# Kernel optimization log

Measured on AMD Instinct MI355X. Metric: run time of the kernel, lower is better.

## Reference

```python
import jax, jax.numpy as jnp
import numpy as np

NHEAD, HEAD_DIM = 10, 10
TEMPERATURE = 1.0
INV_SQRT_HD = np.float32(1.0 / np.sqrt(HEAD_DIM))


def setup_inputs() -> dict:
    key = jax.random.key(0)
    ks = jax.random.split(key, 6)
    B, nhid, L = 4, 128, 1024
    D = NHEAD * HEAD_DIM  # 100
    x = jax.random.normal(ks[0], (B, nhid, L, 1), dtype=jnp.float32)
    edge_matrix = jax.random.randint(ks[1], (B, L, L), 0, 2, dtype=jnp.int32)
    wq_w = jax.random.normal(ks[2], (D, nhid), dtype=jnp.float32) * 0.05
    wq_b = jnp.zeros((D,), jnp.float32)
    wedge_w = jax.random.normal(ks[3], (2 * HEAD_DIM,), dtype=jnp.float32) * 0.1
    wedge_b = jnp.zeros((1,), jnp.float32)
    wo_w = jax.random.normal(ks[4], (nhid, D), dtype=jnp.float32) * 0.05
    wo_b = jnp.zeros((nhid,), jnp.float32)
    return dict(x=x, edge_matrix=edge_matrix, wq_w=wq_w, wq_b=wq_b,
                wedge_w=wedge_w, wedge_b=wedge_b, wo_w=wo_w, wo_b=wo_b)


def reference(x, edge_matrix, wq_w, wq_b, wedge_w, wedge_b, wo_w, wo_b):
    B, nhid, L, _ = x.shape
    # WQ: 1x1 conv == per-position linear over channels
    q = jnp.einsum('bhl,ch->bcl', x[..., 0], wq_w) + wq_b[None, :, None]  # (B, nhead*hd, L)
    # source overwrites k and v with q (WK/WV dead code): k == v == q
    k = q.reshape(B, NHEAD, HEAD_DIM, L).transpose(0, 1, 3, 2)  # (B, nhead, L, hd)
    # WEDGE(Linear(2*hd,1)) over concat[k_i, k_j] == w1.k_i + w2.k_j + b (exact same math,
    # avoids materializing the O(L^2 * 2*hd) a_input tensor)
    s_i = jnp.einsum('bnld,d->bnl', k, wedge_w[:HEAD_DIM])
    s_j = jnp.einsum('bnld,d->bnl', k, wedge_w[HEAD_DIM:])
    alpha = (s_i[:, :, :, None] + s_j[:, :, None, :] + wedge_b[0]) * INV_SQRT_HD  # (B,nhead,L,L)
    alpha = jnp.where(edge_matrix[:, None, :, :] == 0, jnp.float32(-1e15), alpha)
    alpha = jax.nn.softmax(alpha, axis=-1) / TEMPERATURE  # dropout: identity at eval
    att = jnp.einsum('bnij,bnjd->bnid', alpha, k)  # v == k; (B, nhead, L, hd)
    # faithful to torch: raw row-major view(B, -1, L, 1) that scrambles (head,pos) ordering
    att = att.reshape(B, NHEAD * HEAD_DIM, L, 1)
    ret = jnp.einsum('bcl,oc->bol', att[..., 0], wo_w) + wo_b[None, :, None]
    ret = ret[..., None]  # (B, nhid, L, 1)
    return ret, alpha.reshape(B * NHEAD, L, L)
```

## Files before the change

### kernel.cpp

```cpp
#include <hip/hip_runtime.h>

#define BB   4
#define NHID 128
#define LL   1024
#define NH   10
#define HD   10
#define DD   100
#define SCALE 0.31622776601683794f

typedef float vfloat4 __attribute__((ext_vector_type(4)));

__global__ __launch_bounds__(256) void k_qproj(
    const float* __restrict__ x, const float* __restrict__ wq_w,
    const float* __restrict__ wq_b, float* __restrict__ kT) {
  const int l  = blockIdx.x * 256 + threadIdx.x;
  const int c0 = blockIdx.y * 2;
  const int b  = blockIdx.z;
  float acc0 = wq_b[c0], acc1 = wq_b[c0 + 1];
  const float* xb = x + (size_t)b * NHID * LL + l;
  const float* w0 = wq_w + (size_t)c0 * NHID;
  const float* w1 = w0 + NHID;
  #pragma unroll 8
  for (int h = 0; h < NHID; ++h) {
    float xv = xb[(size_t)h * LL];
    acc0 += w0[h] * xv;
    acc1 += w1[h] * xv;
  }
  {
    int c = c0, n = c / HD, d = c % HD;
    kT[(((size_t)(b * NH + n)) * HD + d) * LL + l] = acc0;
  }
  {
    int c = c0 + 1, n = c / HD, d = c % HD;
    kT[(((size_t)(b * NH + n)) * HD + d) * LL + l] = acc1;
  }
}

__global__ __launch_bounds__(256) void k_edgeproj(
    const float* __restrict__ kT, const float* __restrict__ we_w,
    float* __restrict__ esj) {
  const int idx = blockIdx.x * 256 + threadIdx.x;
  const int bn = idx >> 10, l = idx & (LL - 1);
  const float* kp = kT + (size_t)bn * HD * LL + l;
  float s2 = 0.f;
  #pragma unroll
  for (int d = 0; d < HD; ++d) s2 += kp[(size_t)d * LL] * we_w[HD + d];
  esj[idx] = __expf(s2 * SCALE);
}

__global__ __launch_bounds__(512) void k_attn(
    const float* __restrict__ kT, const float* __restrict__ esj,
    const int* __restrict__ edge,
    float* __restrict__ alpha_out, float* __restrict__ att) {
  const int t    = threadIdx.x;
  const int lane = t & 63;
  const int wid  = t >> 6;
  const int blk  = blockIdx.x;
  const int rt   = blk & 31;
  const int bn   = blk >> 5;
  const int b    = bn / NH;
  const int i0   = rt * 32 + wid * 4;

  __shared__ float ksT[HD * LL];
  {
    const float4* src = (const float4*)(kT + (size_t)bn * (HD * LL));
    float4* dst = (float4*)ksT;
    #pragma unroll
    for (int idx = t; idx < (HD * LL) / 4; idx += 512) dst[idx] = src[idx];
  }
  vfloat4 esv[4];
  {
    const vfloat4* sp = (const vfloat4*)(esj + (size_t)bn * LL);
    #pragma unroll
    for (int m = 0; m < 4; ++m) esv[m] = sp[m * 64 + lane];
  }
  __syncthreads();

  const int* ebase = edge + (size_t)b * LL * LL + (size_t)i0 * LL;

  float part[4][HD];
  float denom[4];
  unsigned mask[4];
  #pragma unroll
  for (int r = 0; r < 4; ++r) {
    denom[r] = 0.f; mask[r] = 0u;
    #pragma unroll
    for (int d = 0; d < HD; ++d) part[r][d] = 0.f;
  }
  #pragma unroll
  for (int m = 0; m < 4; ++m) {
    vfloat4 kv[HD];
    const float* kb = ksT + m * 256 + lane * 4;
    #pragma unroll
    for (int d = 0; d < HD; ++d) kv[d] = *(const vfloat4*)(kb + d * LL);
    const vfloat4 es = esv[m];
    #pragma unroll
    for (int r = 0; r < 4; ++r) {
      int4 e = ((const int4*)(ebase + (size_t)r * LL))[m * 64 + lane];
      float ax = e.x ? es.x : 0.f;
      float ay = e.y ? es.y : 0.f;
      float az = e.z ? es.z : 0.f;
      float aw = e.w ? es.w : 0.f;
      mask[r] |= ((e.x ? 1u : 0u) | (e.y ? 2u : 0u) | (e.z ? 4u : 0u) | (e.w ? 8u : 0u)) << (m * 4);
      denom[r] += (ax + ay) + (az + aw);
      #pragma unroll
      for (int d = 0; d < HD; ++d)
        part[r][d] += ax * kv[d].x + ay * kv[d].y + az * kv[d].z + aw * kv[d].w;
    }
  }
  float inv[4];
  #pragma unroll
  for (int r = 0; r < 4; ++r) {
    float s = denom[r];
    #pragma unroll
    for (int sft = 32; sft >= 1; sft >>= 1) s += __shfl_xor(s, sft, 64);
    inv[r] = __builtin_amdgcn_rcpf(s);
  }

  float* ap = alpha_out + ((size_t)bn * LL + i0) * LL;
  #pragma unroll
  for (int m = 0; m < 4; ++m) {
    const vfloat4 es = esv[m];
    #pragma unroll
    for (int r = 0; r < 4; ++r) {
      const unsigned mk = mask[r] >> (m * 4);
      vfloat4 a;
      a.x = (mk & 1u) ? es.x * inv[r] : 0.f;
      a.y = (mk & 2u) ? es.y * inv[r] : 0.f;
      a.z = (mk & 4u) ? es.z * inv[r] : 0.f;
      a.w = (mk & 8u) ? es.w * inv[r] : 0.f;
      vfloat4* dst = (vfloat4*)(ap + (size_t)r * LL) + m * 64 + lane;
      __builtin_nontemporal_store(a, dst);
    }
  }

  const bool b5 = (lane & 32) != 0;
  const bool b4 = (lane & 16) != 0;
  const bool b3 = (lane & 8) != 0;
  const bool b2 = (lane & 4) != 0;
  #pragma unroll
  for (int r = 0; r < 4; ++r) {
    float pv[16];
    #pragma unroll
    for (int d = 0; d < HD; ++d) pv[d] = part[r][d];
    #pragma unroll
    for (int d = HD; d < 16; ++d) pv[d] = 0.f;
    #pragma unroll
    for (int i = 0; i < 8; ++i) {
      float snd = b5 ? pv[i] : pv[i + 8];
      float kp  = b5 ? pv[i + 8] : pv[i];
      pv[i] = kp + __shfl_xor(snd, 32, 64);
    }
    #pragma unroll
    for (int i = 0; i < 4; ++i) {
      float snd = b4 ? pv[i] : pv[i + 4];
      float kp  = b4 ? pv[i + 4] : pv[i];
      pv[i] = kp + __shfl_xor(snd, 16, 64);
    }
    #pragma unroll
    for (int i = 0; i < 2; ++i) {
      float snd = b3 ? pv[i] : pv[i + 2];
      float kp  = b3 ? pv[i + 2] : pv[i];
      pv[i] = kp + __shfl_xor(snd, 8, 64);
    }
    {
      float snd = b2 ? pv[0] : pv[1];
      float kp  = b2 ? pv[1] : pv[0];
      pv[0] = kp + __shfl_xor(snd, 4, 64);
    }
    pv[0] += __shfl_xor(pv[0], 2, 64);
    pv[0] += __shfl_xor(pv[0], 1, 64);
    float g = __shfl(pv[0], lane * 4, 64);
    if (lane < HD)
      att[((size_t)bn * LL + (i0 + r)) * HD + lane] = g * inv[r];
  }
}

__global__ __launch_bounds__(256) void k_out(
    const float* __restrict__ att, const float* __restrict__ wo_w,
    const float* __restrict__ wo_b, float* __restrict__ ret) {
  const int l  = blockIdx.x * 256 + threadIdx.x;
  const int o0 = blockIdx.y * 4;
  const int b  = blockIdx.z;
  const float* ab = att + (size_t)b * (DD * LL);
  float acc[4];
  #pragma unroll
  for (int oo = 0; oo < 4; ++oo) acc[oo] = wo_b[o0 + oo];
  for (int c = 0; c < DD; ++c) {
    float a = ab[(size_t)c * LL + l];
    #pragma unroll
    for (int oo = 0; oo < 4; ++oo) acc[oo] += wo_w[(size_t)(o0 + oo) * DD + c] * a;
  }
  #pragma unroll
  for (int oo = 0; oo < 4; ++oo)
    ret[((size_t)b * NHID + o0 + oo) * LL + l] = acc[oo];
}

extern "C" void kernel_launch(void* const* d_in, const int* in_sizes, int n_in,
                              void* d_out, int out_size, void* d_ws, size_t ws_size,
                              hipStream_t stream) {
  (void)in_sizes; (void)n_in; (void)out_size; (void)ws_size;
  const float* x    = (const float*)d_in[0];
  const int*   edge = (const int*)d_in[1];
  const float* wq_w = (const float*)d_in[2];
  const float* wq_b = (const float*)d_in[3];
  const float* we_w = (const float*)d_in[4];
  const float* wo_w = (const float*)d_in[6];
  const float* wo_b = (const float*)d_in[7];

  float* out       = (float*)d_out;
  float* ret_out   = out;
  float* alpha_out = out + (size_t)BB * NHID * LL;

  float* ws   = (float*)d_ws;
  float* kT   = ws;
  float* esj  = kT + (size_t)BB * NH * HD * LL;
  float* att  = esj + (size_t)BB * NH * LL;

  dim3 g1(LL / 256, DD / 2, BB);
  k_qproj<<<g1, 256, 0, stream>>>(x, wq_w, wq_b, kT);

  k_edgeproj<<<(BB * NH * LL) / 256, 256, 0, stream>>>(kT, we_w, esj);

  k_attn<<<BB * NH * (LL / 32), 512, 0, stream>>>(kT, esj, edge, alpha_out, att);

  dim3 g3(LL / 256, NHID / 4, BB);
  k_out<<<g3, 256, 0, stream>>>(att, wo_w, wo_b, ret_out);
}
```

Before: 255.3 us.

## Process two heads per attention block to reuse edge mask loads

The attention kernel now handles two heads per block. It loads the edge matrix rows once into a bitmask and reuses that mask for both heads, which halves global reads of the large int32 edge tensor. Shared memory per block doubles to 80KB and launch bounds now request 3 blocks per CU, which may reduce occupancy. The Q projection also computes 4 output channels per thread instead of 2, cutting repeated reads of x.

New measurement: 356.3 us. +39.6%, slower.

```diff
diff --git a/kernel.cpp b/kernel.cpp
--- a/kernel.cpp
+++ b/kernel.cpp
@@ -14,25 +14,23 @@
     const float* __restrict__ x, const float* __restrict__ wq_w,
     const float* __restrict__ wq_b, float* __restrict__ kT) {
   const int l  = blockIdx.x * 256 + threadIdx.x;
-  const int c0 = blockIdx.y * 2;
+  const int c0 = blockIdx.y * 4;
   const int b  = blockIdx.z;
-  float acc0 = wq_b[c0], acc1 = wq_b[c0 + 1];
+  float acc[4];
+  #pragma unroll
+  for (int i = 0; i < 4; ++i) acc[i] = wq_b[c0 + i];
   const float* xb = x + (size_t)b * NHID * LL + l;
   const float* w0 = wq_w + (size_t)c0 * NHID;
-  const float* w1 = w0 + NHID;
-  #pragma unroll 8
+  #pragma unroll 4
   for (int h = 0; h < NHID; ++h) {
     float xv = xb[(size_t)h * LL];
-    acc0 += w0[h] * xv;
-    acc1 += w1[h] * xv;
-  }
-  {
-    int c = c0, n = c / HD, d = c % HD;
-    kT[(((size_t)(b * NH + n)) * HD + d) * LL + l] = acc0;
-  }
-  {
-    int c = c0 + 1, n = c / HD, d = c % HD;
-    kT[(((size_t)(b * NH + n)) * HD + d) * LL + l] = acc1;
+    #pragma unroll
+    for (int i = 0; i < 4; ++i) acc[i] += w0[i * NHID + h] * xv;
+  }
+  #pragma unroll
+  for (int i = 0; i < 4; ++i) {
+    int c = c0 + i, n = c / HD, d = c % HD;
+    kT[(((size_t)(b * NH + n)) * HD + d) * LL + l] = acc[i];
   }
 }
 
@@ -48,131 +46,154 @@
   esj[idx] = __expf(s2 * SCALE);
 }
 
-__global__ __launch_bounds__(512) void k_attn(
+__device__ __forceinline__ void pv_reduce_store(
+    float part[4][HD], const float* inv, float* __restrict__ att,
+    int bn, int i0, int lane) {
+  const bool c5 = (lane & 32) != 0;
+  const bool c4 = (lane & 16) != 0;
+  const bool c3 = (lane & 8) != 0;
+  const bool c2 = (lane & 4) != 0;
+  #pragma unroll
+  for (int r = 0; r < 4; ++r) {
+    float pv[16];
+    #pragma unroll
+    for (int d = 0; d < HD; ++d) pv[d] = part[r][d];
+    #pragma unroll
+    for (int d = HD; d < 16; ++d) pv[d] = 0.f;
+    #pragma unroll
+    for (int i = 0; i < 8; ++i) {
+      float snd = c5 ? pv[i] : pv[i + 8];
+      float kp  = c5 ? pv[i + 8] : pv[i];
+      pv[i] = kp + __shfl_xor(snd, 32, 64);
+    }
+    #pragma unroll
+    for (int i = 0; i < 4; ++i) {
+      float snd = c4 ? pv[i] : pv[i + 4];
+      float kp  = c4 ? pv[i + 4] : pv[i];
+      pv[i] = kp + __shfl_xor(snd, 16, 64);
+    }
+    #pragma unroll
+    for (int i = 0; i < 2; ++i) {
+      float snd = c3 ? pv[i] : pv[i + 2];
+      float kp  = c3 ? pv[i + 2] : pv[i];
+      pv[i] = kp + __shfl_xor(snd, 8, 64);
+    }
+    {
+      float snd = c2 ? pv[0] : pv[1];
+      float kp  = c2 ? pv[1] : pv[0];
+      pv[0] = kp + __shfl_xor(snd, 4, 64);
+    }
+    pv[0] += __shfl_xor(pv[0], 2, 64);
+    pv[0] += __shfl_xor(pv[0], 1, 64);
+    float g = __shfl(pv[0], lane * 4, 64);
+    if (lane < HD)
+      att[((size_t)bn * LL + (i0 + r)) * HD + lane] = g * inv[r];
+  }
+}
+
+__global__ __launch_bounds__(512, 3) void k_attn(
     const float* __restrict__ kT, const float* __restrict__ esj,
     const int* __restrict__ edge,
     float* __restrict__ alpha_out, float* __restrict__ att) {
   const int t    = threadIdx.x;
   const int lane = t & 63;
   const int wid  = t >> 6;
-  const int blk  = blockIdx.x;
-  const int rt   = blk & 31;
-  const int bn   = blk >> 5;
-  const int b    = bn / NH;
+  const int rt   = blockIdx.x;
+  const int hp   = blockIdx.y;
+  const int b    = blockIdx.z;
+  const int bn0  = b * NH + hp * 2;
   const int i0   = rt * 32 + wid * 4;
 
-  __shared__ float ksT[HD * LL];
+  __shared__ float ksT2[2 * HD * LL];
   {
-    const float4* src = (const float4*)(kT + (size_t)bn * (HD * LL));
-    float4* dst = (float4*)ksT;
-    #pragma unroll
-    for (int idx = t; idx < (HD * LL) / 4; idx += 512) dst[idx] = src[idx];
-  }
-  vfloat4 esv[4];
+    const float4* src = (const float4*)(kT + (size_t)bn0 * (HD * LL));
+    float4* dst = (float4*)ksT2;
+    #pragma unroll
+    for (int idx = t; idx < (2 * HD * LL) / 4; idx += 512) dst[idx] = src[idx];
+  }
+  vfloat4 esv[2][4];
   {
-    const vfloat4* sp = (const vfloat4*)(esj + (size_t)bn * LL);
-    #pragma unroll
-    for (int m = 0; m < 4; ++m) esv[m] = sp[m * 64 + lane];
+    #pragma unroll
+    for (int h = 0; h < 2; ++h) {
+      const vfloat4* sp = (const vfloat4*)(esj + (size_t)(bn0 + h) * LL);
+      #pragma unroll
+      for (int m = 0; m < 4; ++m) esv[h][m] = sp[m * 64 + lane];
+    }
   }
   __syncthreads();
 
   const int* ebase = edge + (size_t)b * LL * LL + (size_t)i0 * LL;
-
-  float part[4][HD];
-  float denom[4];
-  unsigned mask[4];
-  #pragma unroll
-  for (int r = 0; r < 4; ++r) {
-    denom[r] = 0.f; mask[r] = 0u;
-    #pragma unroll
-    for (int d = 0; d < HD; ++d) part[r][d] = 0.f;
-  }
+  unsigned mask[4] = {0u, 0u, 0u, 0u};
   #pragma unroll
   for (int m = 0; m < 4; ++m) {
-    vfloat4 kv[HD];
-    const float* kb = ksT + m * 256 + lane * 4;
-    #pragma unroll
-    for (int d = 0; d < HD; ++d) kv[d] = *(const vfloat4*)(kb + d * LL);
-    const vfloat4 es = esv[m];
     #pragma unroll
     for (int r = 0; r < 4; ++r) {
       int4 e = ((const int4*)(ebase + (size_t)r * LL))[m * 64 + lane];
-      float ax = e.x ? es.x : 0.f;
-      float ay = e.y ? es.y : 0.f;
-      float az = e.z ? es.z : 0.f;
-      float aw = e.w ? es.w : 0.f;
-      mask[r] |= ((e.x ? 1u : 0u) | (e.y ? 2u : 0u) | (e.z ? 4u : 0u) | (e.w ? 8u : 0u)) << (m * 4);
-      denom[r] += (ax + ay) + (az + aw);
-      #pragma unroll
-      for (int d = 0; d < HD; ++d)
-        part[r][d] += ax * kv[d].x + ay * kv[d].y + az * kv[d].z + aw * kv[d].w;
-    }
-  }
-  float inv[4];
-  #pragma unroll
-  for (int r = 0; r < 4; ++r) {
-    float s = denom[r];
-    #pragma unroll
-    for (int sft = 32; sft >= 1; sft >>= 1) s += __shfl_xor(s, sft, 64);
-    inv[r] = __builtin_amdgcn_rcpf(s);
-  }
-
-  float* ap = alpha_out + ((size_t)bn * LL + i0) * LL;
-  #pragma unroll
-  for (int m = 0; m < 4; ++m) {
-    const vfloat4 es = esv[m];
+      mask[r] |= ((e.x ? 1u : 0u) | (e.y ? 2u : 0u) |
+                  (e.z ? 4u : 0u) | (e.w ? 8u : 0u)) << (m * 4);
+    }
+  }
+
+  #pragma unroll
+  for (int h = 0; h < 2; ++h) {
+    const int bn = bn0 + h;
+    const float* ksT = ksT2 + h * (HD * LL);
+
+    float part[4][HD];
+    float denom[4];
     #pragma unroll
     for (int r = 0; r < 4; ++r) {
-      const unsigned mk = mask[r] >> (m * 4);
-      vfloat4 a;
-      a.x = (mk & 1u) ? es.x * inv[r] : 0.f;
-      a.y = (mk & 2u) ? es.y * inv[r] : 0.f;
-      a.z = (mk & 4u) ? es.z * inv[r] : 0.f;
-      a.w = (mk & 8u) ? es.w * inv[r] : 0.f;
-      vfloat4* dst = (vfloat4*)(ap + (size_t)r * LL) + m * 64 + lane;
-      __builtin_nontemporal_store(a, dst);
-    }
-  }
-
-  const bool b5 = (lane & 32) != 0;
-  const bool b4 = (lane & 16) != 0;
-  const bool b3 = (lane & 8) != 0;
-  const bool b2 = (lane & 4) != 0;
-  #pragma unroll
-  for (int r = 0; r < 4; ++r) {
-    float pv[16];
-    #pragma unroll
-    for (int d = 0; d < HD; ++d) pv[d] = part[r][d];
-    #pragma unroll
-    for (int d = HD; d < 16; ++d) pv[d] = 0.f;
-    #pragma unroll
-    for (int i = 0; i < 8; ++i) {
-      float snd = b5 ? pv[i] : pv[i + 8];
-      float kp  = b5 ? pv[i + 8] : pv[i];
-      pv[i] = kp + __shfl_xor(snd, 32, 64);
-    }
-    #pragma unroll
-    for (int i = 0; i < 4; ++i) {
-      float snd = b4 ? pv[i] : pv[i + 4];
-      float kp  = b4 ? pv[i + 4] : pv[i];
-      pv[i] = kp + __shfl_xor(snd, 16, 64);
-    }
-    #pragma unroll
-    for (int i = 0; i < 2; ++i) {
-      float snd = b3 ? pv[i] : pv[i + 2];
-      float kp  = b3 ? pv[i + 2] : pv[i];
-      pv[i] = kp + __shfl_xor(snd, 8, 64);
-    }
-    {
-      float snd = b2 ? pv[0] : pv[1];
-      float kp  = b2 ? pv[1] : pv[0];
-      pv[0] = kp + __shfl_xor(snd, 4, 64);
-    }
-    pv[0] += __shfl_xor(pv[0], 2, 64);
-    pv[0] += __shfl_xor(pv[0], 1, 64);
-    float g = __shfl(pv[0], lane * 4, 64);
-    if (lane < HD)
-      att[((size_t)bn * LL + (i0 + r)) * HD + lane] = g * inv[r];
+      denom[r] = 0.f;
+      #pragma unroll
+      for (int d = 0; d < HD; ++d) part[r][d] = 0.f;
+    }
+    #pragma unroll
+    for (int m = 0; m < 4; ++m) {
+      vfloat4 kv[HD];
+      const float* kb = ksT + m * 256 + lane * 4;
+      #pragma unroll
+      for (int d = 0; d < HD; ++d) kv[d] = *(const vfloat4*)(kb + d * LL);
+      const vfloat4 es = esv[h][m];
+      #pragma unroll
+      for (int r = 0; r < 4; ++r) {
+        const unsigned mk = mask[r] >> (m * 4);
+        float ax = (mk & 1u) ? es.x : 0.f;
+        float ay = (mk & 2u) ? es.y : 0.f;
+        float az = (mk & 4u) ? es.z : 0.f;
+        float aw = (mk & 8u) ? es.w : 0.f;
+        denom[r] += (ax + ay) + (az + aw);
+        #pragma unroll
+        for (int d = 0; d < HD; ++d)
+          part[r][d] += ax * kv[d].x + ay * kv[d].y + az * kv[d].z + aw * kv[d].w;
+      }
+    }
+    float inv[4];
+    #pragma unroll
+    for (int r = 0; r < 4; ++r) {
+      float s = denom[r];
+      #pragma unroll
+      for (int sft = 32; sft >= 1; sft >>= 1) s += __shfl_xor(s, sft, 64);
+      inv[r] = __builtin_amdgcn_rcpf(s);
+    }
+
+    float* ap = alpha_out + ((size_t)bn * LL + i0) * LL;
+    #pragma unroll
+    for (int m = 0; m < 4; ++m) {
+      const vfloat4 es = esv[h][m];
+      #pragma unroll
+      for (int r = 0; r < 4; ++r) {
+        const unsigned mk = mask[r] >> (m * 4);
+        vfloat4 a;
+        a.x = (mk & 1u) ? es.x * inv[r] : 0.f;
+        a.y = (mk & 2u) ? es.y * inv[r] : 0.f;
+        a.z = (mk & 4u) ? es.z * inv[r] : 0.f;
+        a.w = (mk & 8u) ? es.w * inv[r] : 0.f;
+        vfloat4* dst = (vfloat4*)(ap + (size_t)r * LL) + m * 64 + lane;
+        __builtin_nontemporal_store(a, dst);
+      }
+    }
+
+    pv_reduce_store(part, inv, att, bn, i0, lane);
   }
 }
 
@@ -217,12 +238,13 @@
   float* esj  = kT + (size_t)BB * NH * HD * LL;
   float* att  = esj + (size_t)BB * NH * LL;
 
-  dim3 g1(LL / 256, DD / 2, BB);
+  dim3 g1(LL / 256, DD / 4, BB);
   k_qproj<<<g1, 256, 0, stream>>>(x, wq_w, wq_b, kT);
 
   k_edgeproj<<<(BB * NH * LL) / 256, 256, 0, stream>>>(kT, we_w, esj);
 
-  k_attn<<<BB * NH * (LL / 32), 512, 0, stream>>>(kT, esj, edge, alpha_out, att);
+  dim3 g2(LL / 32, NH / 2, BB);
+  k_attn<<<g2, 512, 0, stream>>>(kT, esj, edge, alpha_out, att);
 
   dim3 g3(LL / 256, NHID / 4, BB);
   k_out<<<g3, 256, 0, stream>>>(att, wo_w, wo_b, ret_out);
```
